# Kernel tuning notes

Measured on AMD Instinct MI355X. Metric: run time of the kernel, lower is better.

Reference implementation:

```python
import jax, jax.numpy as jnp
import numpy as np

N = 65536
APP = 1024
SP = 512
HID = 512
CARD = 16
SUB = HID // CARD  # 32


def setup_inputs() -> dict:
    key = jax.random.key(0)
    ks = jax.random.split(key, 8)
    s1 = 1.0 / np.sqrt(APP)
    s2 = 1.0 / np.sqrt(SP)
    s3 = 1.0 / np.sqrt(SUB)
    return {
        "appearance": jax.random.normal(ks[0], (N, APP), jnp.float32),
        "spatial": jax.random.normal(ks[1], (N, SP), jnp.float32),
        # Batched per-branch weights (torch Linear: y = x @ W.T + b; here stored as [in, out])
        "W1": jax.random.uniform(ks[2], (CARD, APP, SUB), jnp.float32, -s1, s1),
        "b1": jax.random.uniform(ks[3], (CARD, SUB), jnp.float32, -s1, s1),
        "W2": jax.random.uniform(ks[4], (CARD, SP, SUB), jnp.float32, -s2, s2),
        "b2": jax.random.uniform(ks[5], (CARD, SP if False else SUB), jnp.float32, -s2, s2),
        "W3": jax.random.uniform(ks[6], (CARD, SUB, HID), jnp.float32, -s3, s3),
        "b3": jax.random.uniform(ks[7], (CARD, HID), jnp.float32, -s3, s3),
    }


def reference(appearance, spatial, W1, b1, W2, b2, W3, b3):
    # fc1[c] = appearance @ W1[c] + b1[c]; fc2[c] = spatial @ W2[c] + b2[c]
    h1 = jnp.einsum('na,cas->ncs', appearance, W1) + b1[None]  # [N, C, SUB]
    h2 = jnp.einsum('np,cps->ncs', spatial, W2) + b2[None]     # [N, C, SUB]
    h = jax.nn.relu(h1 + h2)
    # sum over branches of (h[:,c] @ W3[c] + b3[c]) == einsum + sum of biases
    out = jnp.einsum('ncs,csh->nh', h, W3) + jnp.sum(b3, axis=0)[None]  # [N, HID]
    return jax.nn.relu(out)
```

## Files before the change

### kernel.cpp

```cpp
#include <hip/hip_runtime.h>

typedef __attribute__((ext_vector_type(4))) float floatx4;
typedef __attribute__((ext_vector_type(8))) short bf16x8;

__device__ __forceinline__ unsigned short f2bf(float f) {
    union { float f; unsigned u; } v; v.f = f;
    unsigned r = v.u + 0x7fffu + ((v.u >> 16) & 1u);
    return (unsigned short)(r >> 16);
}

__global__ void prep_kernel(const float* __restrict__ W1, const float* __restrict__ b1,
                            const float* __restrict__ W2, const float* __restrict__ b2,
                            const float* __restrict__ W3, const float* __restrict__ b3,
                            unsigned short* __restrict__ wcat, unsigned short* __restrict__ w3f,
                            float* __restrict__ bias12, float* __restrict__ bias3s)
{
    int tid = blockIdx.x * 256 + threadIdx.x;
    if (tid < 98304) {
        int l  = tid & 63;
        int nt = (tid >> 6) & 31;
        int kc = tid >> 11;
        int n  = nt * 16 + (l & 15);
        int k0 = kc * 32 + ((l >> 4) << 3);
        int c = n >> 5, s = n & 31;
        union { unsigned short us[8]; int4 v; } pk;
        const float* src = (k0 < 1024) ? (W1 + c * 32768 + k0 * 32 + s)
                                       : (W2 + c * 16384 + (k0 - 1024) * 32 + s);
        #pragma unroll
        for (int j = 0; j < 8; ++j) pk.us[j] = f2bf(src[j * 32]);
        *(int4*)(wcat + (size_t)tid * 8) = pk.v;
    } else if (tid < 131072) {
        int t  = tid - 98304;
        int l  = t & 63;
        int nt = (t >> 6) & 31;
        int kc = t >> 11;
        int n  = nt * 16 + (l & 15);
        int k0 = kc * 32 + ((l >> 4) << 3);
        union { unsigned short us[8]; int4 v; } pk;
        const float* src = W3 + k0 * 512 + n;
        #pragma unroll
        for (int j = 0; j < 8; ++j) pk.us[j] = f2bf(src[j * 512]);
        *(int4*)(w3f + (size_t)t * 8) = pk.v;
    } else if (tid < 131584) {
        int n = tid - 131072;
        bias12[n] = b1[n] + b2[n];
        float sacc = 0.f;
        #pragma unroll
        for (int c = 0; c < 16; ++c) sacc += b3[c * 512 + n];
        bias3s[n] = sacc;
    }
}

__global__ __launch_bounds__(256, 2) void fused_main(
    const float* __restrict__ app, const float* __restrict__ sp,
    const unsigned short* __restrict__ wcat, const unsigned short* __restrict__ w3f,
    const float* __restrict__ bias12, const float* __restrict__ bias3s,
    float* __restrict__ out)
{
    __shared__ unsigned short As[2][4][64][8];
    __shared__ unsigned short Hf[4][16][64][8];

    const int tid = (int)threadIdx.x;
    const int w   = tid >> 6;
    const int l   = tid & 63;
    const int rowbase = (int)blockIdx.x * 64;

    const int sr  = tid >> 2;
    const int scc = tid & 3;
    const float* appsrc = app + (size_t)(rowbase + sr) * 1024 + scc * 8;
    const float* spsrc  = sp  + (size_t)(rowbase + sr) * 512  + scc * 8;
    unsigned short* as0 = &As[0][sr >> 4][scc * 16 + (sr & 15)][0];
    unsigned short* as1 = &As[1][sr >> 4][scc * 16 + (sr & 15)][0];

    floatx4 acc[4][8];
    #pragma unroll
    for (int mt = 0; mt < 4; ++mt)
        #pragma unroll
        for (int nt = 0; nt < 8; ++nt)
            acc[mt][nt] = (floatx4){0.f, 0.f, 0.f, 0.f};

    {
        float4 p0 = *(const float4*)(appsrc);
        float4 p1 = *(const float4*)(appsrc + 4);
        union { unsigned short us[8]; int4 v; } pk;
        pk.us[0] = f2bf(p0.x); pk.us[1] = f2bf(p0.y); pk.us[2] = f2bf(p0.z); pk.us[3] = f2bf(p0.w);
        pk.us[4] = f2bf(p1.x); pk.us[5] = f2bf(p1.y); pk.us[6] = f2bf(p1.z); pk.us[7] = f2bf(p1.w);
        *(int4*)as0 = pk.v;
    }

    for (int kb = 0; kb < 48; ++kb) {
        __syncthreads();
        const int buf = kb & 1;
        float4 p0, p1;
        if (kb + 1 < 48) {
            const float* src = (kb + 1 < 32) ? (appsrc + (kb + 1) * 32)
                                             : (spsrc + (kb + 1 - 32) * 32);
            p0 = *(const float4*)(src);
            p1 = *(const float4*)(src + 4);
        }
        bf16x8 bfrag[8];
        #pragma unroll
        for (int nt = 0; nt < 8; ++nt)
            bfrag[nt] = *(const bf16x8*)(wcat + (((size_t)kb * 32 + w * 8 + nt) * 64 + l) * 8);
        bf16x8 afrag[4];
        #pragma unroll
        for (int mt = 0; mt < 4; ++mt)
            afrag[mt] = *(const bf16x8*)(&As[buf][mt][l][0]);
        #pragma unroll
        for (int mt = 0; mt < 4; ++mt)
            #pragma unroll
            for (int nt = 0; nt < 8; ++nt)
                acc[mt][nt] = __builtin_amdgcn_mfma_f32_16x16x32_bf16(
                    afrag[mt], bfrag[nt], acc[mt][nt], 0, 0, 0);
        if (kb + 1 < 48) {
            union { unsigned short us[8]; int4 v; } pk;
            pk.us[0] = f2bf(p0.x); pk.us[1] = f2bf(p0.y); pk.us[2] = f2bf(p0.z); pk.us[3] = f2bf(p0.w);
            pk.us[4] = f2bf(p1.x); pk.us[5] = f2bf(p1.y); pk.us[6] = f2bf(p1.z); pk.us[7] = f2bf(p1.w);
            *(int4*)((buf == 0) ? as1 : as0) = pk.v;
        }
    }

    #pragma unroll
    for (int nt = 0; nt < 8; ++nt) {
        const int colg = w * 128 + nt * 16 + (l & 15);
        const float bv = bias12[colg];
        const int kc  = colg >> 5;
        const int lhi = ((colg >> 3) & 3) << 4;
        const int j   = colg & 7;
        #pragma unroll
        for (int mt = 0; mt < 4; ++mt)
            #pragma unroll
            for (int r = 0; r < 4; ++r) {
                const int rlow = ((l >> 4) << 2) + r;
                float v = acc[mt][nt][r] + bv;
                v = fmaxf(v, 0.f);
                Hf[mt][kc][lhi + rlow][j] = f2bf(v);
            }
    }
    __syncthreads();

    #pragma unroll
    for (int mt = 0; mt < 4; ++mt)
        #pragma unroll
        for (int nt = 0; nt < 8; ++nt)
            acc[mt][nt] = (floatx4){0.f, 0.f, 0.f, 0.f};

    for (int kc = 0; kc < 16; ++kc) {
        bf16x8 bfrag[8];
        #pragma unroll
        for (int nt = 0; nt < 8; ++nt)
            bfrag[nt] = *(const bf16x8*)(w3f + (((size_t)kc * 32 + w * 8 + nt) * 64 + l) * 8);
        bf16x8 afrag[4];
        #pragma unroll
        for (int mt = 0; mt < 4; ++mt)
            afrag[mt] = *(const bf16x8*)(&Hf[mt][kc][l][0]);
        #pragma unroll
        for (int mt = 0; mt < 4; ++mt)
            #pragma unroll
            for (int nt = 0; nt < 8; ++nt)
                acc[mt][nt] = __builtin_amdgcn_mfma_f32_16x16x32_bf16(
                    afrag[mt], bfrag[nt], acc[mt][nt], 0, 0, 0);
    }

    #pragma unroll
    for (int nt = 0; nt < 8; ++nt) {
        const int colg = w * 128 + nt * 16 + (l & 15);
        const float bv = bias3s[colg];
        #pragma unroll
        for (int mt = 0; mt < 4; ++mt)
            #pragma unroll
            for (int r = 0; r < 4; ++r) {
                const int rowg = mt * 16 + ((l >> 4) << 2) + r;
                float v = acc[mt][nt][r] + bv;
                v = fmaxf(v, 0.f);
                out[(size_t)(rowbase + rowg) * 512 + colg] = v;
            }
    }
}

extern "C" void kernel_launch(void* const* d_in, const int* in_sizes, int n_in,
                              void* d_out, int out_size, void* d_ws, size_t ws_size,
                              hipStream_t stream)
{
    const float* app = (const float*)d_in[0];
    const float* sp  = (const float*)d_in[1];
    const float* W1  = (const float*)d_in[2];
    const float* b1  = (const float*)d_in[3];
    const float* W2  = (const float*)d_in[4];
    const float* b2  = (const float*)d_in[5];
    const float* W3  = (const float*)d_in[6];
    const float* b3  = (const float*)d_in[7];

    char* ws = (char*)d_ws;
    unsigned short* wcat  = (unsigned short*)(ws);
    unsigned short* w3f   = (unsigned short*)(ws + 1572864);
    float*          b12   = (float*)(ws + 2097152);
    float*          b3s   = (float*)(ws + 2099200);

    prep_kernel<<<514, 256, 0, stream>>>(W1, b1, W2, b2, W3, b3, wcat, w3f, b12, b3s);

    float* outp = (float*)d_out;
    fused_main<<<65536 / 64, 256, 0, stream>>>(app, sp, wcat, w3f, b12, b3s, outp);
}
```

Before: 577.9 us.

## Use 512-thread blocks with 8 waves each owning 64 output columns

```diff
diff --git a/kernel.cpp b/kernel.cpp
--- a/kernel.cpp
+++ b/kernel.cpp
@@ -51,7 +51,7 @@
     }
 }
 
-__global__ __launch_bounds__(256, 2) void fused_main(
+__global__ __launch_bounds__(512, 4) void fused_main(
     const float* __restrict__ app, const float* __restrict__ sp,
     const unsigned short* __restrict__ wcat, const unsigned short* __restrict__ w3f,
     const float* __restrict__ bias12, const float* __restrict__ bias3s,
@@ -65,43 +65,42 @@
     const int l   = tid & 63;
     const int rowbase = (int)blockIdx.x * 64;
 
-    const int sr  = tid >> 2;
-    const int scc = tid & 3;
-    const float* appsrc = app + (size_t)(rowbase + sr) * 1024 + scc * 8;
-    const float* spsrc  = sp  + (size_t)(rowbase + sr) * 512  + scc * 8;
-    unsigned short* as0 = &As[0][sr >> 4][scc * 16 + (sr & 15)][0];
-    unsigned short* as1 = &As[1][sr >> 4][scc * 16 + (sr & 15)][0];
-
-    floatx4 acc[4][8];
+    const int sr  = tid >> 3;
+    const int scc = tid & 7;
+    const float* appsrc = app + (size_t)(rowbase + sr) * 1024 + scc * 4;
+    const float* spsrc  = sp  + (size_t)(rowbase + sr) * 512  + scc * 4;
+    unsigned short* as0 = &As[0][sr >> 4][(scc >> 1) * 16 + (sr & 15)][(scc & 1) * 4];
+    unsigned short* as1 = &As[1][sr >> 4][(scc >> 1) * 16 + (sr & 15)][(scc & 1) * 4];
+
+    floatx4 acc[4][4];
     #pragma unroll
     for (int mt = 0; mt < 4; ++mt)
         #pragma unroll
-        for (int nt = 0; nt < 8; ++nt)
+        for (int nt = 0; nt < 4; ++nt)
             acc[mt][nt] = (floatx4){0.f, 0.f, 0.f, 0.f};
 
     {
-        float4 p0 = *(const float4*)(appsrc);
-        float4 p1 = *(const float4*)(appsrc + 4);
-        union { unsigned short us[8]; int4 v; } pk;
-        pk.us[0] = f2bf(p0.x); pk.us[1] = f2bf(p0.y); pk.us[2] = f2bf(p0.z); pk.us[3] = f2bf(p0.w);
-        pk.us[4] = f2bf(p1.x); pk.us[5] = f2bf(p1.y); pk.us[6] = f2bf(p1.z); pk.us[7] = f2bf(p1.w);
-        *(int4*)as0 = pk.v;
-    }
+        float4 p = *(const float4*)(appsrc);
+        union { unsigned short us[4]; int2 v; } pk;
+        pk.us[0] = f2bf(p.x); pk.us[1] = f2bf(p.y);
+        pk.us[2] = f2bf(p.z); pk.us[3] = f2bf(p.w);
+        *(int2*)as0 = pk.v;
+    }
+    float4 pA = *(const float4*)(appsrc + 32);
 
     for (int kb = 0; kb < 48; ++kb) {
         __syncthreads();
         const int buf = kb & 1;
-        float4 p0, p1;
-        if (kb + 1 < 48) {
-            const float* src = (kb + 1 < 32) ? (appsrc + (kb + 1) * 32)
-                                             : (spsrc + (kb + 1 - 32) * 32);
-            p0 = *(const float4*)(src);
-            p1 = *(const float4*)(src + 4);
+        float4 pB;
+        if (kb + 2 < 48) {
+            const float* src = (kb + 2 < 32) ? (appsrc + (kb + 2) * 32)
+                                             : (spsrc + (kb + 2 - 32) * 32);
+            pB = *(const float4*)src;
         }
-        bf16x8 bfrag[8];
-        #pragma unroll
-        for (int nt = 0; nt < 8; ++nt)
-            bfrag[nt] = *(const bf16x8*)(wcat + (((size_t)kb * 32 + w * 8 + nt) * 64 + l) * 8);
+        bf16x8 bfrag[4];
+        #pragma unroll
+        for (int nt = 0; nt < 4; ++nt)
+            bfrag[nt] = *(const bf16x8*)(wcat + (((size_t)kb * 32 + w * 4 + nt) * 64 + l) * 8);
         bf16x8 afrag[4];
         #pragma unroll
         for (int mt = 0; mt < 4; ++mt)
@@ -109,20 +108,21 @@
         #pragma unroll
         for (int mt = 0; mt < 4; ++mt)
             #pragma unroll
-            for (int nt = 0; nt < 8; ++nt)
+            for (int nt = 0; nt < 4; ++nt)
                 acc[mt][nt] = __builtin_amdgcn_mfma_f32_16x16x32_bf16(
                     afrag[mt], bfrag[nt], acc[mt][nt], 0, 0, 0);
         if (kb + 1 < 48) {
-            union { unsigned short us[8]; int4 v; } pk;
-            pk.us[0] = f2bf(p0.x); pk.us[1] = f2bf(p0.y); pk.us[2] = f2bf(p0.z); pk.us[3] = f2bf(p0.w);
-            pk.us[4] = f2bf(p1.x); pk.us[5] = f2bf(p1.y); pk.us[6] = f2bf(p1.z); pk.us[7] = f2bf(p1.w);
-            *(int4*)((buf == 0) ? as1 : as0) = pk.v;
+            union { unsigned short us[4]; int2 v; } pk;
+            pk.us[0] = f2bf(pA.x); pk.us[1] = f2bf(pA.y);
+            pk.us[2] = f2bf(pA.z); pk.us[3] = f2bf(pA.w);
+            *(int2*)((buf == 0) ? as1 : as0) = pk.v;
+            pA = pB;
         }
     }
 
     #pragma unroll
-    for (int nt = 0; nt < 8; ++nt) {
-        const int colg = w * 128 + nt * 16 + (l & 15);
+    for (int nt = 0; nt < 4; ++nt) {
+        const int colg = w * 64 + nt * 16 + (l & 15);
         const float bv = bias12[colg];
         const int kc  = colg >> 5;
         const int lhi = ((colg >> 3) & 3) << 4;
@@ -142,14 +142,14 @@
     #pragma unroll
     for (int mt = 0; mt < 4; ++mt)
         #pragma unroll
-        for (int nt = 0; nt < 8; ++nt)
+        for (int nt = 0; nt < 4; ++nt)
             acc[mt][nt] = (floatx4){0.f, 0.f, 0.f, 0.f};
 
     for (int kc = 0; kc < 16; ++kc) {
-        bf16x8 bfrag[8];
-        #pragma unroll
-        for (int nt = 0; nt < 8; ++nt)
-            bfrag[nt] = *(const bf16x8*)(w3f + (((size_t)kc * 32 + w * 8 + nt) * 64 + l) * 8);
+        bf16x8 bfrag[4];
+        #pragma unroll
+        for (int nt = 0; nt < 4; ++nt)
+            bfrag[nt] = *(const bf16x8*)(w3f + (((size_t)kc * 32 + w * 4 + nt) * 64 + l) * 8);
         bf16x8 afrag[4];
         #pragma unroll
         for (int mt = 0; mt < 4; ++mt)
@@ -157,14 +157,14 @@
         #pragma unroll
         for (int mt = 0; mt < 4; ++mt)
             #pragma unroll
-            for (int nt = 0; nt < 8; ++nt)
+            for (int nt = 0; nt < 4; ++nt)
                 acc[mt][nt] = __builtin_amdgcn_mfma_f32_16x16x32_bf16(
                     afrag[mt], bfrag[nt], acc[mt][nt], 0, 0, 0);
     }
 
     #pragma unroll
-    for (int nt = 0; nt < 8; ++nt) {
-        const int colg = w * 128 + nt * 16 + (l & 15);
+    for (int nt = 0; nt < 4; ++nt) {
+        const int colg = w * 64 + nt * 16 + (l & 15);
         const float bv = bias3s[colg];
         #pragma unroll
         for (int mt = 0; mt < 4; ++mt)
@@ -200,5 +200,5 @@
     prep_kernel<<<514, 256, 0, stream>>>(W1, b1, W2, b2, W3, b3, wcat, w3f, b12, b3s);
 
     float* outp = (float*)d_out;
-    fused_main<<<65536 / 64, 256, 0, stream>>>(app, sp, wcat, w3f, b12, b3s, outp);
-}
+    fused_main<<<65536 / 64, 512, 0, stream>>>(app, sp, wcat, w3f, b12, b3s, outp);
+}
```

New measurement: 564.0 us. 2.4% less time.
